# Kernel optimization log

Hardware: AMD Instinct MI355X
Metric: run time of the kernel (lower is better)

The kernel has to match this reference:

```python
import jax, jax.numpy as jnp
import numpy as np

B, S, E, D = 256, 256, 2, 128  # batch, seq_len, encoder_dim, decoder_dim


def setup_inputs() -> dict:
    key = jax.random.key(0)
    ks = jax.random.split(key, 9)
    u = lambda k, shape, n: jax.random.uniform(k, shape, jnp.float32, -1.0 / np.sqrt(n), 1.0 / np.sqrt(n))
    return {
        "out_encoder": jax.random.normal(ks[0], (B, S, E), jnp.float32),
        "W1_w": u(ks[1], (S, S), S),            # Linear(seq_len, seq_len)
        "W1_b": u(ks[2], (S,), S),
        "W2_w": u(ks[3], (S, 2 * S), 2 * S),    # Linear(2*seq_len, seq_len)
        "W2_b": u(ks[4], (S,), 2 * S),
        "W_ih": u(ks[5], (4 * D, E), D),        # LSTMCell input weights (i,f,g,o)
        "W_hh": u(ks[6], (4 * D, D), D),
        "b_ih": u(ks[7], (4 * D,), D),
        "b_hh": u(ks[8], (4 * D,), D),
    }


def reference(out_encoder, W1_w, W1_b, W2_w, W2_b, W_ih, W_hh, b_ih, b_hh):
    b, s, e = out_encoder.shape
    d = W_hh.shape[1]
    dt = out_encoder.dtype

    # W_2 term: encoder flattened to [B, 2S]; identical every step, hoist it.
    w2term = out_encoder.reshape(b, s * e) @ W2_w.T + W2_b          # [B, S]
    # W_1 applied to a row of S copies of h_d equals h_d * rowsum(W1) + b.
    w1sum = W1_w.sum(axis=1)                                        # [S]

    def attn(h):  # h: [B, D] -> context [B, E]
        hterm = h[:, :, None] * w1sum[None, None, :] + W1_b         # [B, D, S]
        en = jnp.tanh(w2term[:, None, :] + hterm)                   # [B, D, S]
        alpha = jax.nn.softmax(en, axis=-1).mean(axis=1)            # [B, S] (softmax over seq)
        return jnp.einsum('bs,bse->be', alpha, out_encoder)         # [B, E]

    def lstm_cell(x, h, c):
        gates = x @ W_ih.T + h @ W_hh.T + b_ih + b_hh               # [B, 4D]
        i, f, g, o = jnp.split(gates, 4, axis=-1)
        c = jax.nn.sigmoid(f) * c + jax.nn.sigmoid(i) * jnp.tanh(g)
        h = jax.nn.sigmoid(o) * jnp.tanh(c)
        return h, c

    h0 = jnp.zeros((b, d), dt)
    c0 = jnp.zeros((b, d), dt)

    def step(carry, _):
        h, c = carry
        x = attn(h)
        h, c = lstm_cell(x, h, c)
        return (h, c), h

    _, hs = jax.lax.scan(step, (h0, c0), None, length=s)
    return hs  # [S, B, D]: stacked decoder hidden states (original returns a list of h_t)
```

## Files before the change

kernel.cpp:

```cpp
#include <hip/hip_runtime.h>

#define NB 256
#define NS 256
#define NE 2
#define ND 128
#define NT 512
#define NN 16
#define RING 32
#define SLOT 144
#define SLOTH 160

typedef float vf4 __attribute__((ext_vector_type(4)));
typedef _Float16 f16x2 __attribute__((ext_vector_type(2)));

constexpr float L2E = 1.4426950408889634f;
constexpr float PI_F = 3.14159265358979323846f;

__device__ const float CT[16][16] = {
 {1,0,0,0,0,0,0,0,0,0,0,0,0,0,0,0},
 {0,1,0,0,0,0,0,0,0,0,0,0,0,0,0,0},
 {-1,0,2,0,0,0,0,0,0,0,0,0,0,0,0,0},
 {0,-3,0,4,0,0,0,0,0,0,0,0,0,0,0,0},
 {1,0,-8,0,8,0,0,0,0,0,0,0,0,0,0,0},
 {0,5,0,-20,0,16,0,0,0,0,0,0,0,0,0,0},
 {-1,0,18,0,-48,0,32,0,0,0,0,0,0,0,0,0},
 {0,-7,0,56,0,-112,0,64,0,0,0,0,0,0,0,0},
 {1,0,-32,0,160,0,-256,0,128,0,0,0,0,0,0,0},
 {0,9,0,-120,0,432,0,-576,0,256,0,0,0,0,0,0},
 {-1,0,50,0,-400,0,1120,0,-1280,0,512,0,0,0,0,0},
 {0,-11,0,220,0,-1232,0,2816,0,-2816,0,1024,0,0,0,0},
 {1,0,-72,0,840,0,-3584,0,6912,0,-6144,0,2048,0,0,0},
 {0,13,0,-364,0,2912,0,-9984,0,16640,0,-13312,0,4096,0,0},
 {-1,0,98,0,-1568,0,9408,0,-26880,0,39424,0,-28672,0,8192,0},
 {0,-15,0,560,0,-6048,0,28800,0,-70400,0,92160,0,-61440,0,16384}};

template <int C>
__device__ __forceinline__ float dppadd(float x) {
    return x + __builtin_bit_cast(float,
        __builtin_amdgcn_update_dpp(0, __builtin_bit_cast(int, x), C, 0xF, 0xF, true));
}
__device__ __forceinline__ float red_quad(float x) {
    x = dppadd<0xB1>(x); x = dppadd<0x4E>(x); return x;
}
__device__ __forceinline__ float red_oct(float x) {
    x = dppadd<0xB1>(x); x = dppadd<0x4E>(x); x = dppadd<0x141>(x); return x;
}
__device__ __forceinline__ float red_wave64(float x) {
    x = dppadd<0xB1>(x); x = dppadd<0x4E>(x); x = dppadd<0x141>(x);
    x = dppadd<0x140>(x); x = dppadd<0x142>(x); x = dppadd<0x143>(x); return x;
}
__device__ __forceinline__ float red_half32(float x) {
    x = dppadd<0xB1>(x); x = dppadd<0x4E>(x); x = dppadd<0x141>(x);
    x = dppadd<0x140>(x); x = dppadd<0x142>(x); return x;
}
__device__ __forceinline__ float red_grp16(float x) {
    x = dppadd<0x141>(x); x = dppadd<0x140>(x);
    x = dppadd<0x142>(x); x = dppadd<0x143>(x); return x;
}

__global__ __launch_bounds__(NT, 2)
void attn_lstm_decoder(const float* __restrict__ enc,
                       const float* __restrict__ W1w,
                       const float* __restrict__ W1b,
                       const float* __restrict__ W2w,
                       const float* __restrict__ W2b,
                       const float* __restrict__ Wih,
                       const float* __restrict__ Whh,
                       const float* __restrict__ bih,
                       const float* __restrict__ bhh,
                       float* __restrict__ out)
{
    const int b    = blockIdx.x;
    const int t    = threadIdx.x;
    const int wave = t >> 6;
    const int lane = t & 63;
    const int g    = t >> 2;
    const int q    = t & 3;
    const bool qb0 = q & 1;
    const bool qb1 = q & 2;
    const int half = lane >> 5;
    const int idx  = lane & 31;
    const int jnode = 2 * wave + half;

    __shared__ __align__(16) float    hist[RING * SLOT];
    __shared__ __align__(16) _Float16 hist16[RING * SLOTH];
    __shared__ __align__(16) float xwbuf[2][16];
    __shared__ float A2_l[NS];
    __shared__ float g2_l[NS];
    __shared__ float e0_l[NS];
    __shared__ float e1_l[NS];
    __shared__ float Ml[NN * NN];
    __shared__ float2 Pn[NN];
    __shared__ float2 Vl[NN];
    __shared__ float Pm0[NN], Pm1[NN];

    {
        float v = enc[b * (NS * NE) + t];
        if (t & 1) e1_l[t >> 1] = v; else e0_l[t >> 1] = v;
    }
    if (t < NN * NN) {
        const int mi = t >> 4, mj = t & 15;
        const float w = (mi == 0) ? (1.0f / NN) : (2.0f / NN);
        Ml[t] = w * __cosf((float)(mi * (2 * mj + 1)) * (PI_F / (2 * NN)));
    }
    __syncthreads();

    for (int r = 0; r < 32; ++r) {
        const int s = wave * 32 + r;
        float p = W1w[s * NS + lane]       + W1w[s * NS + lane + 64]
                + W1w[s * NS + lane + 128] + W1w[s * NS + lane + 192];
        p = red_wave64(p);
        if (lane == 63) g2_l[s] = p * (2.0f * L2E);
        float qq = 0.0f;
        #pragma unroll
        for (int kk = 0; kk < 8; ++kk) {
            const int c = lane + kk * 64;
            const float ev = (c & 1) ? e1_l[c >> 1] : e0_l[c >> 1];
            qq = fmaf(ev, W2w[s * (2 * NS) + c], qq);
        }
        qq = red_wave64(qq);
        if (lane == 63) A2_l[s] = (qq + W2b[s] + W1b[s]) * (2.0f * L2E);
    }
    __syncthreads();

    {
        const float y  = __cosf((float)(2 * jnode + 1) * (PI_F / (2 * NN)));
        const float C2 = -2.0f * L2E;
        float l = 0.0f, p0 = 0.0f, p1 = 0.0f;
        #pragma unroll
        for (int k = 0; k < 8; ++k) {
            const int s = k * 32 + idx;
            const float m1 = fmaf(y, g2_l[s], A2_l[s]);
            const float u  = __builtin_amdgcn_exp2f(m1);
            const float rc = __builtin_amdgcn_rcpf(u + 1.0f);
            const float e  = __builtin_amdgcn_exp2f(rc * C2);
            l += e;
            p0 = fmaf(e, e0_l[s], p0);
            p1 = fmaf(e, e1_l[s], p1);
        }
        l = red_half32(l); p0 = red_half32(p0); p1 = red_half32(p1);
        if ((lane & 31) == 31) {
            const float rl = __builtin_amdgcn_rcpf(l);
            Pn[jnode] = make_float2(p0 * rl, p1 * rl);
        }
    }
    __syncthreads();

    if (t < NN) {
        float v0 = 0.0f, v1 = 0.0f;
        #pragma unroll
        for (int j = 0; j < NN; ++j) {
            v0 = fmaf(Ml[t * NN + j], Pn[j].x, v0);
            v1 = fmaf(Ml[t * NN + j], Pn[j].y, v1);
        }
        Vl[t] = make_float2(v0 * (1.0f / ND), v1 * (1.0f / ND));
    }

    f16x2 wr16[4][16];
    float wi0_[4], wi1_[4], bb_[4];
    #pragma unroll
    for (int j = 0; j < 4; ++j) {
        const int r = g + 128 * j;
        const vf4* W4 = reinterpret_cast<const vf4*>(Whh + r * ND + q * 32);
        #pragma unroll
        for (int i = 0; i < 8; ++i) {
            const vf4 w = W4[i];
            wr16[j][2 * i + 0] = f16x2{(_Float16)w.x, (_Float16)w.y};
            wr16[j][2 * i + 1] = f16x2{(_Float16)w.z, (_Float16)w.w};
        }
        wi0_[j] = Wih[r * 2 + 0];
        wi1_[j] = Wih[r * 2 + 1];
        bb_[j]  = bih[r] + bhh[r];
    }

    if (t < ND) {
        hist[31 * SLOT + 36 * (t >> 5) + (t & 31)] = 0.0f;
        hist16[31 * SLOTH + 40 * (t >> 5) + (t & 31)] = (_Float16)0.0f;
    }
    float h_reg = 0.0f, c_reg = 0.0f;
    __syncthreads();

    if (t < NN) {
        float s0 = 0.0f, s1 = 0.0f;
        #pragma unroll
        for (int k = 0; k < NN; ++k) {
            s0 = fmaf(Vl[k].x, CT[k][t], s0);
            s1 = fmaf(Vl[k].y, CT[k][t], s1);
        }
        Pm0[t] = s0; Pm1[t] = s1;
    }
    __syncthreads();

    float Q0[4], Q1[4];
    #pragma unroll
    for (int i = 0; i < 4; ++i) { Q0[i] = Pm0[4 * i + q]; Q1[i] = Pm1[4 * i + q]; }

    auto phaseG = [&](float h, int pw) {
        const float h2 = h * h;
        const float h3 = h2 * h;
        const float h4 = h2 * h2;
        const float hq = qb1 ? (qb0 ? h3 : h2) : (qb0 ? h : 1.0f);
        float a0 = fmaf(Q0[3], h4, Q0[2]);
        a0 = fmaf(a0, h4, Q0[1]);
        a0 = fmaf(a0, h4, Q0[0]);
        float a1 = fmaf(Q1[3], h4, Q1[2]);
        a1 = fmaf(a1, h4, Q1[1]);
        a1 = fmaf(a1, h4, Q1[0]);
        a0 *= hq;
        a1 *= hq;
        a0 = red_quad(a0);  a1 = red_quad(a1);
        a0 = red_grp16(a0); a1 = red_grp16(a1);
        if (lane == 63) {
            xwbuf[pw][2 * wave + 0] = a0;
            xwbuf[pw][2 * wave + 1] = a1;
        }
    };

    phaseG(0.0f, 0);
    __syncthreads();

    for (int step = 0; step < NS; ++step) {
        const int pr = step & 1;
        const int rs = (step + RING - 1) & (RING - 1);
        const int ws = step & (RING - 1);

        float2 xv = *reinterpret_cast<const float2*>(&xwbuf[pr][2 * (lane & 7)]);
        const int4* hb = reinterpret_cast<const int4*>(&hist16[rs * SLOTH + q * 40]);
        int hw[16];
        #pragma unroll
        for (int i = 0; i < 4; ++i) {
            const int4 v = hb[i];
            hw[4 * i + 0] = v.x; hw[4 * i + 1] = v.y;
            hw[4 * i + 2] = v.z; hw[4 * i + 3] = v.w;
        }

        if ((step & 15) == 0 && step > 0) {
            const int sb  = (step - 16) & (RING - 1);
            const int k   = t >> 5;
            const int l32 = t & 31;
            const int w   = 4 * l32;
            const vf4 v = *reinterpret_cast<const vf4*>(
                &hist[(sb + k) * SLOT + 36 * (w >> 5) + (w & 31)]);
            *reinterpret_cast<vf4*>(
                &out[(size_t)(step - 16 + k) * (NB * ND) + b * ND + w]) = v;
        }

        float x0 = red_oct(xv.x);
        float x1 = red_oct(xv.y);

        float d0a = 0.f, d0b = 0.f, d1a = 0.f, d1b = 0.f;
        float d2a = 0.f, d2b = 0.f, d3a = 0.f, d3b = 0.f;
        #pragma unroll
        for (int i = 0; i < 8; ++i) {
            const f16x2 ha = __builtin_bit_cast(f16x2, hw[2 * i + 0]);
            const f16x2 hbv = __builtin_bit_cast(f16x2, hw[2 * i + 1]);
            d0a = __builtin_amdgcn_fdot2(wr16[0][2 * i + 0], ha,  d0a, false);
            d0b = __builtin_amdgcn_fdot2(wr16[0][2 * i + 1], hbv, d0b, false);
            d1a = __builtin_amdgcn_fdot2(wr16[1][2 * i + 0], ha,  d1a, false);
            d1b = __builtin_amdgcn_fdot2(wr16[1][2 * i + 1], hbv, d1b, false);
            d2a = __builtin_amdgcn_fdot2(wr16[2][2 * i + 0], ha,  d2a, false);
            d2b = __builtin_amdgcn_fdot2(wr16[2][2 * i + 1], hbv, d2b, false);
            d3a = __builtin_amdgcn_fdot2(wr16[3][2 * i + 0], ha,  d3a, false);
            d3b = __builtin_amdgcn_fdot2(wr16[3][2 * i + 1], hbv, d3b, false);
        }
        float d0 = d0a + d0b, d1 = d1a + d1b;
        float d2 = d2a + d2b, d3 = d3a + d3b;
        d0 = red_quad(d0);  d1 = red_quad(d1);
        d2 = red_quad(d2);  d3 = red_quad(d3);

        const float gi = d0 + fmaf(x0, wi0_[0], fmaf(x1, wi1_[0], bb_[0]));
        const float gf = d1 + fmaf(x0, wi0_[1], fmaf(x1, wi1_[1], bb_[1]));
        const float gg = d2 + fmaf(x0, wi0_[2], fmaf(x1, wi1_[2], bb_[2]));
        const float go = d3 + fmaf(x0, wi0_[3], fmaf(x1, wi1_[3], bb_[3]));

        const float si = __builtin_amdgcn_rcpf(1.0f + __builtin_amdgcn_exp2f(-L2E * gi));
        const float sf = __builtin_amdgcn_rcpf(1.0f + __builtin_amdgcn_exp2f(-L2E * gf));
        const float so = __builtin_amdgcn_rcpf(1.0f + __builtin_amdgcn_exp2f(-L2E * go));
        const float tg = 1.0f - 2.0f * __builtin_amdgcn_rcpf(__builtin_amdgcn_exp2f(2.0f * L2E * gg) + 1.0f);
        c_reg = sf * c_reg + si * tg;
        const float tc2 = 1.0f - 2.0f * __builtin_amdgcn_rcpf(__builtin_amdgcn_exp2f(2.0f * L2E * c_reg) + 1.0f);
        h_reg = so * tc2;

        if (q == 0) {
            hist[ws * SLOT + 36 * (g >> 5) + (g & 31)] = h_reg;
            hist16[ws * SLOTH + 40 * (g >> 5) + (g & 31)] = (_Float16)h_reg;
        }
        phaseG(h_reg, pr ^ 1);

        __syncthreads();
    }

    {
        const int k   = t >> 5;
        const int l32 = t & 31;
        const int w   = 4 * l32;
        const vf4 v = *reinterpret_cast<const vf4*>(
            &hist[(16 + k) * SLOT + 36 * (w >> 5) + (w & 31)]);
        *reinterpret_cast<vf4*>(
            &out[(size_t)(240 + k) * (NB * ND) + b * ND + w]) = v;
    }
}

extern "C" void kernel_launch(void* const* d_in, const int* in_sizes, int n_in,
                              void* d_out, int out_size, void* d_ws, size_t ws_size,
                              hipStream_t stream) {
    const float* enc = (const float*)d_in[0];
    const float* W1w = (const float*)d_in[1];
    const float* W1b = (const float*)d_in[2];
    const float* W2w = (const float*)d_in[3];
    const float* W2b = (const float*)d_in[4];
    const float* Wih = (const float*)d_in[5];
    const float* Whh = (const float*)d_in[6];
    const float* bih = (const float*)d_in[7];
    const float* bhh = (const float*)d_in[8];
    attn_lstm_decoder<<<NB, NT, 0, stream>>>(enc, W1w, W1b, W2w, W2b,
                                             Wih, Whh, bih, bhh, (float*)d_out);
}
```

Measured before the change: 299.5 us.

## Double threads per block to split each gate row across eight lanes

Raises the block size from 512 to 1024 threads, so each LSTM gate row is handled by eight lanes instead of four. This halves the fp16 Whh weights held in registers per thread and halves the serial dot-product chain per step. Every dependent piece is re-laid out to match: the hist16 padding, the Chebyshev polynomial split, the DPP reductions, the x-projection buffer and the output copy. The aim is a shorter critical path in each serial recurrence step, at the cost of an extra reduction level and a heavier barrier across 16 waves.

New measurement: 395.7 us. 32.1% more time.

```diff
diff --git a/kernel.cpp b/kernel.cpp
--- a/kernel.cpp
+++ b/kernel.cpp
@@ -4,11 +4,11 @@
 #define NS 256
 #define NE 2
 #define ND 128
-#define NT 512
+#define NT 1024
 #define NN 16
 #define RING 32
 #define SLOT 144
-#define SLOTH 160
+#define SLOTH 192
 
 typedef float vf4 __attribute__((ext_vector_type(4)));
 typedef _Float16 f16x2 __attribute__((ext_vector_type(2)));
@@ -39,26 +39,22 @@
     return x + __builtin_bit_cast(float,
         __builtin_amdgcn_update_dpp(0, __builtin_bit_cast(int, x), C, 0xF, 0xF, true));
 }
-__device__ __forceinline__ float red_quad(float x) {
-    x = dppadd<0xB1>(x); x = dppadd<0x4E>(x); return x;
-}
 __device__ __forceinline__ float red_oct(float x) {
     x = dppadd<0xB1>(x); x = dppadd<0x4E>(x); x = dppadd<0x141>(x); return x;
+}
+__device__ __forceinline__ float red_row16(float x) {
+    x = dppadd<0xB1>(x); x = dppadd<0x4E>(x); x = dppadd<0x141>(x);
+    x = dppadd<0x140>(x); return x;
 }
 __device__ __forceinline__ float red_wave64(float x) {
     x = dppadd<0xB1>(x); x = dppadd<0x4E>(x); x = dppadd<0x141>(x);
     x = dppadd<0x140>(x); x = dppadd<0x142>(x); x = dppadd<0x143>(x); return x;
 }
-__device__ __forceinline__ float red_half32(float x) {
-    x = dppadd<0xB1>(x); x = dppadd<0x4E>(x); x = dppadd<0x141>(x);
-    x = dppadd<0x140>(x); x = dppadd<0x142>(x); return x;
-}
-__device__ __forceinline__ float red_grp16(float x) {
-    x = dppadd<0x141>(x); x = dppadd<0x140>(x);
-    x = dppadd<0x142>(x); x = dppadd<0x143>(x); return x;
-}
-
-__global__ __launch_bounds__(NT, 2)
+__device__ __forceinline__ float red_oct2wave(float x) {
+    x = dppadd<0x140>(x); x = dppadd<0x142>(x); x = dppadd<0x143>(x); return x;
+}
+
+__global__ __launch_bounds__(NT, 4)
 void attn_lstm_decoder(const float* __restrict__ enc,
                        const float* __restrict__ W1w,
                        const float* __restrict__ W1b,
@@ -74,17 +70,15 @@
     const int t    = threadIdx.x;
     const int wave = t >> 6;
     const int lane = t & 63;
-    const int g    = t >> 2;
-    const int q    = t & 3;
+    const int g    = t >> 3;
+    const int q    = t & 7;
     const bool qb0 = q & 1;
     const bool qb1 = q & 2;
-    const int half = lane >> 5;
-    const int idx  = lane & 31;
-    const int jnode = 2 * wave + half;
+    const bool qb2 = q & 4;
 
     __shared__ __align__(16) float    hist[RING * SLOT];
     __shared__ __align__(16) _Float16 hist16[RING * SLOTH];
-    __shared__ __align__(16) float xwbuf[2][16];
+    __shared__ __align__(16) float xwbuf[2][32];
     __shared__ float A2_l[NS];
     __shared__ float g2_l[NS];
     __shared__ float e0_l[NS];
@@ -94,7 +88,7 @@
     __shared__ float2 Vl[NN];
     __shared__ float Pm0[NN], Pm1[NN];
 
-    {
+    if (t < 512) {
         float v = enc[b * (NS * NE) + t];
         if (t & 1) e1_l[t >> 1] = v; else e0_l[t >> 1] = v;
     }
@@ -105,8 +99,8 @@
     }
     __syncthreads();
 
-    for (int r = 0; r < 32; ++r) {
-        const int s = wave * 32 + r;
+    for (int r = 0; r < 16; ++r) {
+        const int s = wave * 16 + r;
         float p = W1w[s * NS + lane]       + W1w[s * NS + lane + 64]
                 + W1w[s * NS + lane + 128] + W1w[s * NS + lane + 192];
         p = red_wave64(p);
@@ -124,12 +118,12 @@
     __syncthreads();
 
     {
-        const float y  = __cosf((float)(2 * jnode + 1) * (PI_F / (2 * NN)));
+        const float y  = __cosf((float)(2 * wave + 1) * (PI_F / (2 * NN)));
         const float C2 = -2.0f * L2E;
         float l = 0.0f, p0 = 0.0f, p1 = 0.0f;
         #pragma unroll
-        for (int k = 0; k < 8; ++k) {
-            const int s = k * 32 + idx;
+        for (int k = 0; k < 4; ++k) {
+            const int s = k * 64 + lane;
             const float m1 = fmaf(y, g2_l[s], A2_l[s]);
             const float u  = __builtin_amdgcn_exp2f(m1);
             const float rc = __builtin_amdgcn_rcpf(u + 1.0f);
@@ -138,10 +132,10 @@
             p0 = fmaf(e, e0_l[s], p0);
             p1 = fmaf(e, e1_l[s], p1);
         }
-        l = red_half32(l); p0 = red_half32(p0); p1 = red_half32(p1);
-        if ((lane & 31) == 31) {
+        l = red_wave64(l); p0 = red_wave64(p0); p1 = red_wave64(p1);
+        if (lane == 63) {
             const float rl = __builtin_amdgcn_rcpf(l);
-            Pn[jnode] = make_float2(p0 * rl, p1 * rl);
+            Pn[wave] = make_float2(p0 * rl, p1 * rl);
         }
     }
     __syncthreads();
@@ -156,14 +150,14 @@
         Vl[t] = make_float2(v0 * (1.0f / ND), v1 * (1.0f / ND));
     }
 
-    f16x2 wr16[4][16];
+    f16x2 wr16[4][8];
     float wi0_[4], wi1_[4], bb_[4];
     #pragma unroll
     for (int j = 0; j < 4; ++j) {
         const int r = g + 128 * j;
-        const vf4* W4 = reinterpret_cast<const vf4*>(Whh + r * ND + q * 32);
-        #pragma unroll
-        for (int i = 0; i < 8; ++i) {
+        const vf4* W4 = reinterpret_cast<const vf4*>(Whh + r * ND + q * 16);
+        #pragma unroll
+        for (int i = 0; i < 4; ++i) {
             const vf4 w = W4[i];
             wr16[j][2 * i + 0] = f16x2{(_Float16)w.x, (_Float16)w.y};
             wr16[j][2 * i + 1] = f16x2{(_Float16)w.z, (_Float16)w.w};
@@ -175,7 +169,7 @@
 
     if (t < ND) {
         hist[31 * SLOT + 36 * (t >> 5) + (t & 31)] = 0.0f;
-        hist16[31 * SLOTH + 40 * (t >> 5) + (t & 31)] = (_Float16)0.0f;
+        hist16[31 * SLOTH + 24 * (t >> 4) + (t & 15)] = (_Float16)0.0f;
     }
     float h_reg = 0.0f, c_reg = 0.0f;
     __syncthreads();
@@ -191,25 +185,21 @@
     }
     __syncthreads();
 
-    float Q0[4], Q1[4];
-    #pragma unroll
-    for (int i = 0; i < 4; ++i) { Q0[i] = Pm0[4 * i + q]; Q1[i] = Pm1[4 * i + q]; }
+    const float Qa0 = Pm0[q],     Qa1 = Pm1[q];
+    const float Qb0 = Pm0[q + 8], Qb1 = Pm1[q + 8];
 
     auto phaseG = [&](float h, int pw) {
         const float h2 = h * h;
-        const float h3 = h2 * h;
         const float h4 = h2 * h2;
-        const float hq = qb1 ? (qb0 ? h3 : h2) : (qb0 ? h : 1.0f);
-        float a0 = fmaf(Q0[3], h4, Q0[2]);
-        a0 = fmaf(a0, h4, Q0[1]);
-        a0 = fmaf(a0, h4, Q0[0]);
-        float a1 = fmaf(Q1[3], h4, Q1[2]);
-        a1 = fmaf(a1, h4, Q1[1]);
-        a1 = fmaf(a1, h4, Q1[0]);
-        a0 *= hq;
-        a1 *= hq;
-        a0 = red_quad(a0);  a1 = red_quad(a1);
-        a0 = red_grp16(a0); a1 = red_grp16(a1);
+        const float h8 = h4 * h4;
+        const float s1 = qb0 ? h  : 1.0f;
+        const float s2 = qb1 ? h2 : 1.0f;
+        const float s4 = qb2 ? h4 : 1.0f;
+        const float hq = s1 * s2 * s4;
+        float a0 = fmaf(Qb0, h8, Qa0) * hq;
+        float a1 = fmaf(Qb1, h8, Qa1) * hq;
+        a0 = red_oct(a0);      a1 = red_oct(a1);
+        a0 = red_oct2wave(a0); a1 = red_oct2wave(a1);
         if (lane == 63) {
             xwbuf[pw][2 * wave + 0] = a0;
             xwbuf[pw][2 * wave + 1] = a1;
@@ -224,35 +214,34 @@
         const int rs = (step + RING - 1) & (RING - 1);
         const int ws = step & (RING - 1);
 
-        float2 xv = *reinterpret_cast<const float2*>(&xwbuf[pr][2 * (lane & 7)]);
-        const int4* hb = reinterpret_cast<const int4*>(&hist16[rs * SLOTH + q * 40]);
-        int hw[16];
-        #pragma unroll
-        for (int i = 0; i < 4; ++i) {
+        float2 xv = *reinterpret_cast<const float2*>(&xwbuf[pr][2 * (lane & 15)]);
+        const int4* hb = reinterpret_cast<const int4*>(&hist16[rs * SLOTH + q * 24]);
+        int hw[8];
+        #pragma unroll
+        for (int i = 0; i < 2; ++i) {
             const int4 v = hb[i];
             hw[4 * i + 0] = v.x; hw[4 * i + 1] = v.y;
             hw[4 * i + 2] = v.z; hw[4 * i + 3] = v.w;
         }
 
         if ((step & 15) == 0 && step > 0) {
-            const int sb  = (step - 16) & (RING - 1);
-            const int k   = t >> 5;
-            const int l32 = t & 31;
-            const int w   = 4 * l32;
-            const vf4 v = *reinterpret_cast<const vf4*>(
-                &hist[(sb + k) * SLOT + 36 * (w >> 5) + (w & 31)]);
-            *reinterpret_cast<vf4*>(
-                &out[(size_t)(step - 16 + k) * (NB * ND) + b * ND + w]) = v;
-        }
-
-        float x0 = red_oct(xv.x);
-        float x1 = red_oct(xv.y);
+            const int sb = (step - 16) & (RING - 1);
+            const int k  = t >> 6;
+            const int l  = t & 63;
+            const float2 v = *reinterpret_cast<const float2*>(
+                &hist[(sb + k) * SLOT + 36 * (l >> 4) + ((2 * l) & 31)]);
+            *reinterpret_cast<float2*>(
+                &out[(size_t)(step - 16 + k) * (NB * ND) + b * ND + 2 * l]) = v;
+        }
+
+        float x0 = red_row16(xv.x);
+        float x1 = red_row16(xv.y);
 
         float d0a = 0.f, d0b = 0.f, d1a = 0.f, d1b = 0.f;
         float d2a = 0.f, d2b = 0.f, d3a = 0.f, d3b = 0.f;
         #pragma unroll
-        for (int i = 0; i < 8; ++i) {
-            const f16x2 ha = __builtin_bit_cast(f16x2, hw[2 * i + 0]);
+        for (int i = 0; i < 4; ++i) {
+            const f16x2 ha  = __builtin_bit_cast(f16x2, hw[2 * i + 0]);
             const f16x2 hbv = __builtin_bit_cast(f16x2, hw[2 * i + 1]);
             d0a = __builtin_amdgcn_fdot2(wr16[0][2 * i + 0], ha,  d0a, false);
             d0b = __builtin_amdgcn_fdot2(wr16[0][2 * i + 1], hbv, d0b, false);
@@ -265,8 +254,8 @@
         }
         float d0 = d0a + d0b, d1 = d1a + d1b;
         float d2 = d2a + d2b, d3 = d3a + d3b;
-        d0 = red_quad(d0);  d1 = red_quad(d1);
-        d2 = red_quad(d2);  d3 = red_quad(d3);
+        d0 = red_oct(d0);  d1 = red_oct(d1);
+        d2 = red_oct(d2);  d3 = red_oct(d3);
 
         const float gi = d0 + fmaf(x0, wi0_[0], fmaf(x1, wi1_[0], bb_[0]));
         const float gf = d1 + fmaf(x0, wi0_[1], fmaf(x1, wi1_[1], bb_[1]));
@@ -283,7 +272,7 @@
 
         if (q == 0) {
             hist[ws * SLOT + 36 * (g >> 5) + (g & 31)] = h_reg;
-            hist16[ws * SLOTH + 40 * (g >> 5) + (g & 31)] = (_Float16)h_reg;
+            hist16[ws * SLOTH + 24 * (g >> 4) + (g & 15)] = (_Float16)h_reg;
         }
         phaseG(h_reg, pr ^ 1);
 
@@ -291,13 +280,12 @@
     }
 
     {
-        const int k   = t >> 5;
-        const int l32 = t & 31;
-        const int w   = 4 * l32;
-        const vf4 v = *reinterpret_cast<const vf4*>(
-            &hist[(16 + k) * SLOT + 36 * (w >> 5) + (w & 31)]);
-        *reinterpret_cast<vf4*>(
-            &out[(size_t)(240 + k) * (NB * ND) + b * ND + w]) = v;
+        const int k = t >> 6;
+        const int l = t & 63;
+        const float2 v = *reinterpret_cast<const float2*>(
+            &hist[(16 + k) * SLOT + 36 * (l >> 4) + ((2 * l) & 31)]);
+        *reinterpret_cast<float2*>(
+            &out[(size_t)(240 + k) * (NB * ND) + b * ND + 2 * l]) = v;
     }
 }
 
```
